# Kernel optimization log

Measured on AMD Instinct MI355X. Metric: run time of the kernel, lower is better.

The kernel has to match this reference:

```python
import jax, jax.numpy as jnp
import numpy as np

N = 170000      # nodes
E = 2400000     # edges
F_IN = 128      # dataset.num_features
H = 64          # hidden_channels
C = 40          # dataset.num_classes
L = 8           # num_layers
ENTROPY = 1.0   # args.entropy
EPS = 1e-20


def setup_inputs() -> dict:
    key = jax.random.key(0)
    ks = jax.random.split(key, 10)
    x = jax.random.normal(ks[0], (N, F_IN), jnp.float32)
    edge_src = jax.random.randint(ks[1], (E,), 0, N)
    edge_dst = jax.random.randint(ks[2], (E,), 0, N)
    edge_weight = jax.random.uniform(ks[3], (E,), jnp.float32) / 14.0  # ~1/deg scale
    u = jax.random.uniform(ks[4], (N, L + 1), jnp.float32, 1e-6, 1.0 - 1e-6)
    gumbel = -jnp.log(-jnp.log(u))  # standard Gumbel noise for gumbel_softmax
    lin0_w = jax.random.normal(ks[5], (F_IN, H), jnp.float32) / np.float32(np.sqrt(F_IN))
    lin0_b = jnp.zeros((H,), jnp.float32)
    meta_w = jax.random.normal(ks[6], (H, 1), jnp.float32) / np.float32(np.sqrt(H))
    meta_b = jnp.zeros((1,), jnp.float32)
    lin1_w = jax.random.normal(ks[7], (H, C), jnp.float32) / np.float32(np.sqrt(H))
    lin1_b = jnp.zeros((C,), jnp.float32)
    return dict(x=x, edge_weight=edge_weight, gumbel=gumbel,
                lin0_w=lin0_w, lin0_b=lin0_b, meta_w=meta_w, meta_b=meta_b,
                lin1_w=lin1_w, lin1_b=lin1_b,
                edge_src=edge_src, edge_dst=edge_dst)


def reference(x, edge_weight, gumbel, lin0_w, lin0_b, meta_w, meta_b,
              lin1_w, lin1_b, edge_src, edge_dst):
    # input projection + relu (dropout=0 -> no-op)
    x = jnp.maximum(x @ lin0_w + lin0_b, 0.0)  # [N,H]
    xs = [x]
    # GCNII layers with conv.alpha = conv.beta = 0 -> pure edge-weighted
    # scatter-add propagation followed by relu.
    for _ in range(L):
        msg = edge_weight[:, None] * x[edge_src]              # [E,H] gather
        x = jax.ops.segment_sum(msg, edge_dst, num_segments=N)  # [N,H] scatter-add
        x = jnp.maximum(x, 0.0)
        xs.append(x)
    xMat = jnp.stack(xs, axis=1)  # [N, L+1, H] (preds == xMatrix since concat='none')
    # MetaNet: [N, L+1]
    r = jnp.squeeze(xMat @ meta_w, -1) + meta_b[0]
    # get_t: stick-breaking with sigmoid; last column uses t=1 times cumprod
    s = jax.nn.sigmoid(r)                                    # [N, L+1]
    cp_excl = jnp.concatenate(
        [jnp.ones((N, 1), s.dtype), jnp.cumprod(1.0 - s, axis=1)[:, :-1]], axis=1)
    t = s * cp_excl
    t = t.at[:, -1].set(cp_excl[:, -1])
    ent_loss = ENTROPY * (-(jnp.log(t + EPS) * t).sum(1).mean())
    # gumbel_softmax(log(t+eps), tau=1, hard=False)
    tM = jax.nn.softmax(jnp.log(t + EPS) + gumbel, axis=1)   # [N, L+1]
    # layer mixing: [N,1,L+1] @ [N,L+1,H] -> [N,H]
    out = jnp.einsum('nl,nlh->nh', tM, xMat)
    out = out @ lin1_w + lin1_b
    return jax.nn.log_softmax(out, axis=-1), ent_loss
```

## Files before the change

### kernel.cpp

```cpp
#include <hip/hip_runtime.h>
#include <hip/hip_bf16.h>

#define N_NODES 170000
#define N_EDGES 2400000
#define F_IN_   128
#define H_      64
#define C_OUT   40
#define L_LAYERS 8
#define LP1     9
#define EPS_T   1e-20f
#define ROW_ELEMS (LP1 * H_)

typedef unsigned short u16;

__device__ __forceinline__ float bf2f(u16 u) {
    union { unsigned int i; float f; } c; c.i = ((unsigned int)u) << 16; return c.f;
}
__device__ __forceinline__ u16 f2bf(float f) {
    __hip_bfloat16 h = __float2bfloat16(f);
    return *reinterpret_cast<u16*>(&h);
}

__device__ __forceinline__ float waveReduceSum(float v) {
    for (int m = 32; m; m >>= 1) v += __shfl_xor(v, m, 64);
    return v;
}
__device__ __forceinline__ float waveReduceMax(float v) {
    for (int m = 32; m; m >>= 1) v = fmaxf(v, __shfl_xor(v, m, 64));
    return v;
}

__global__ __launch_bounds__(256) void k_zero4(float4* __restrict__ p) {
    p[blockIdx.x * 256 + threadIdx.x] = make_float4(0.f, 0.f, 0.f, 0.f);
}

__global__ __launch_bounds__(256) void k_hist(
    const int* __restrict__ edst, int* __restrict__ deg)
{
    int e = blockIdx.x * 256 + threadIdx.x;
    if (e < N_EDGES) atomicAdd(&deg[edst[e]], 1);
}

#define SCAN_TPB 256
#define SCAN_VPT 8
#define SCAN_EPB (SCAN_TPB * SCAN_VPT)
#define SCAN_BLOCKS ((N_NODES + SCAN_EPB - 1) / SCAN_EPB)

__global__ __launch_bounds__(SCAN_TPB) void k_scan1(
    const int* __restrict__ deg, int* __restrict__ rowstart,
    int* __restrict__ blockSums)
{
    __shared__ int tsum[SCAN_TPB];
    int tid = threadIdx.x;
    int base = blockIdx.x * SCAN_EPB + tid * SCAN_VPT;
    int vals[SCAN_VPT];
    int local = 0;
    #pragma unroll
    for (int i = 0; i < SCAN_VPT; ++i) {
        int idx = base + i;
        int v = (idx < N_NODES) ? deg[idx] : 0;
        vals[i] = local;
        local += v;
    }
    tsum[tid] = local;
    __syncthreads();
    for (int off = 1; off < SCAN_TPB; off <<= 1) {
        int v = (tid >= off) ? tsum[tid - off] : 0;
        __syncthreads();
        tsum[tid] += v;
        __syncthreads();
    }
    int texcl = tsum[tid] - local;
    #pragma unroll
    for (int i = 0; i < SCAN_VPT; ++i) {
        int idx = base + i;
        if (idx < N_NODES) rowstart[idx] = texcl + vals[i];
    }
    if (tid == SCAN_TPB - 1) blockSums[blockIdx.x] = tsum[tid];
}

__global__ __launch_bounds__(64) void k_scan2(int* __restrict__ blockSums) {
    if (threadIdx.x == 0) {
        int acc = 0;
        for (int i = 0; i < SCAN_BLOCKS; ++i) {
            int v = blockSums[i];
            blockSums[i] = acc;
            acc += v;
        }
    }
}

__global__ __launch_bounds__(SCAN_TPB) void k_scan3(
    int* __restrict__ rowstart, const int* __restrict__ blockSums)
{
    int off = blockSums[blockIdx.x];
    int base = blockIdx.x * SCAN_EPB + threadIdx.x * SCAN_VPT;
    #pragma unroll
    for (int i = 0; i < SCAN_VPT; ++i) {
        int idx = base + i;
        if (idx < N_NODES) rowstart[idx] += off;
    }
}

__global__ __launch_bounds__(256) void k_bucket(
    const int* __restrict__ esrc, const int* __restrict__ edst,
    const float* __restrict__ ew, const int* __restrict__ rowstart,
    int* __restrict__ cursor, int2* __restrict__ csr, int lo, int hi)
{
    int e = blockIdx.x * 256 + threadIdx.x;
    if (e >= N_EDGES) return;
    int d = edst[e];
    if (d < lo || d >= hi) return;
    int p = rowstart[d] + atomicAdd(&cursor[d], 1);
    csr[p] = make_int2(esrc[e], __float_as_int(ew[e]));
}

#define L0_NPB 64
__global__ __launch_bounds__(256) void k_lin0(
    const float* __restrict__ x, const float* __restrict__ W0,
    const float* __restrict__ b0, const float* __restrict__ mw,
    const float* __restrict__ mb, u16* __restrict__ xMatB,
    float* __restrict__ r)
{
    __shared__ float Wt[H_ * F_IN_];
    __shared__ float xr[L0_NPB * F_IN_];
    int tid = threadIdx.x;
    for (int i = tid; i < F_IN_ * H_; i += 256) {
        int k = i >> 6, c = i & 63;
        Wt[c * F_IN_ + (k ^ ((c & 7) << 2))] = W0[i];
    }
    int nb = blockIdx.x * L0_NPB;
    const float4* x4 = (const float4*)(x + (size_t)nb * F_IN_);
    float4* xr4 = (float4*)xr;
    int nvalid = N_NODES - nb; if (nvalid > L0_NPB) nvalid = L0_NPB;
    int limit4 = nvalid * (F_IN_ / 4);
    for (int i = tid; i < L0_NPB * (F_IN_ / 4); i += 256)
        xr4[i] = (i < limit4) ? x4[i] : make_float4(0.f, 0.f, 0.f, 0.f);
    __syncthreads();

    int wave = tid >> 6, lane = tid & 63;
    const int mbase = wave * 16;
    float bias = b0[lane];
    float acc[16];
    #pragma unroll
    for (int j = 0; j < 16; ++j) acc[j] = bias;
    const int wrow = lane * F_IN_;
    const int wsw = (lane & 7) << 2;
    for (int k0 = 0; k0 < F_IN_; k0 += 4) {
        float4 wv = *(const float4*)&Wt[wrow + (k0 ^ wsw)];
        #pragma unroll
        for (int j = 0; j < 16; ++j) {
            float4 xv = *(const float4*)&xr[(mbase + j) * F_IN_ + k0];
            acc[j] = fmaf(xv.w, wv.w,
                     fmaf(xv.z, wv.z, fmaf(xv.y, wv.y, fmaf(xv.x, wv.x, acc[j]))));
        }
    }
    float mwv = mw[lane];
    for (int j = 0; j < 16; ++j) {
        int n = nb + mbase + j;
        if (n >= N_NODES) break;
        float v = fmaxf(acc[j], 0.f);
        xMatB[(size_t)n * ROW_ELEMS + lane] = f2bf(v);
        float pr = waveReduceSum(v * mwv);
        if (lane == 0) r[n * LP1] = pr + mb[0];
    }
}

__global__ __launch_bounds__(256) void k_prop(
    const u16* __restrict__ xMatB, int l,
    const int* __restrict__ rowstart, const int* __restrict__ deg,
    const int2* __restrict__ csr,
    const float* __restrict__ mw, const float* __restrict__ mb,
    u16* __restrict__ xMatOut, float* __restrict__ r)
{
    int tid = threadIdx.x, wave = tid >> 6, lane = tid & 63;
    int n = blockIdx.x * 4 + wave;
    int sl = lane & 15, q = lane >> 4;
    int start = rowstart[n];
    int d = deg[n];
    int dm1 = (d > 0) ? (d - 1) : 0;

    int myS = 0; float myW = 0.f;
    if (lane < d) {
        int2 e = csr[start + lane];
        myS = e.x; myW = __int_as_float(e.y);
    }
    const unsigned loff = (unsigned)l * H_ + sl * 4;

    float a0x = 0.f, a0y = 0.f, a0z = 0.f, a0w = 0.f;
    float a1x = 0.f, a1y = 0.f, a1z = 0.f, a1w = 0.f;
    float a2x = 0.f, a2y = 0.f, a2z = 0.f, a2w = 0.f;
    float a3x = 0.f, a3y = 0.f, a3z = 0.f, a3w = 0.f;

    int dmax = (d < 64) ? d : 64;
    int kb = 0;
    do {
        int idx0 = kb + q;
        int idx1 = kb + q + 4;
        int idx2 = kb + q + 8;
        int idx3 = kb + q + 12;
        int ic0 = (idx0 < dm1) ? idx0 : dm1;
        int ic1 = (idx1 < dm1) ? idx1 : dm1;
        int ic2 = (idx2 < dm1) ? idx2 : dm1;
        int ic3 = (idx3 < dm1) ? idx3 : dm1;
        int   s0 = __shfl(myS, ic0, 64); float w0 = __shfl(myW, ic0, 64);
        int   s1 = __shfl(myS, ic1, 64); float w1 = __shfl(myW, ic1, 64);
        int   s2 = __shfl(myS, ic2, 64); float w2 = __shfl(myW, ic2, 64);
        int   s3 = __shfl(myS, ic3, 64); float w3 = __shfl(myW, ic3, 64);
        if (idx0 >= d) w0 = 0.f;
        if (idx1 >= d) w1 = 0.f;
        if (idx2 >= d) w2 = 0.f;
        if (idx3 >= d) w3 = 0.f;
        ushort4 v0 = *reinterpret_cast<const ushort4*>(
            &xMatB[(size_t)(unsigned)s0 * ROW_ELEMS + loff]);
        ushort4 v1 = *reinterpret_cast<const ushort4*>(
            &xMatB[(size_t)(unsigned)s1 * ROW_ELEMS + loff]);
        ushort4 v2 = *reinterpret_cast<const ushort4*>(
            &xMatB[(size_t)(unsigned)s2 * ROW_ELEMS + loff]);
        ushort4 v3 = *reinterpret_cast<const ushort4*>(
            &xMatB[(size_t)(unsigned)s3 * ROW_ELEMS + loff]);
        a0x = fmaf(bf2f(v0.x), w0, a0x); a0y = fmaf(bf2f(v0.y), w0, a0y);
        a0z = fmaf(bf2f(v0.z), w0, a0z); a0w = fmaf(bf2f(v0.w), w0, a0w);
        a1x = fmaf(bf2f(v1.x), w1, a1x); a1y = fmaf(bf2f(v1.y), w1, a1y);
        a1z = fmaf(bf2f(v1.z), w1, a1z); a1w = fmaf(bf2f(v1.w), w1, a1w);
        a2x = fmaf(bf2f(v2.x), w2, a2x); a2y = fmaf(bf2f(v2.y), w2, a2y);
        a2z = fmaf(bf2f(v2.z), w2, a2z); a2w = fmaf(bf2f(v2.w), w2, a2w);
        a3x = fmaf(bf2f(v3.x), w3, a3x); a3y = fmaf(bf2f(v3.y), w3, a3y);
        a3z = fmaf(bf2f(v3.z), w3, a3z); a3w = fmaf(bf2f(v3.w), w3, a3w);
        kb += 16;
    } while (kb < dmax);

    for (int kb2 = 64; kb2 < d; kb2 += 16) {
        #pragma unroll
        for (int j = 0; j < 4; ++j) {
            int idx = kb2 + j * 4 + q;
            if (idx < d) {
                int2 e = csr[start + idx];
                float w = __int_as_float(e.y);
                ushort4 v = *reinterpret_cast<const ushort4*>(
                    &xMatB[(size_t)(unsigned)e.x * ROW_ELEMS + loff]);
                a0x = fmaf(bf2f(v.x), w, a0x);
                a0y = fmaf(bf2f(v.y), w, a0y);
                a0z = fmaf(bf2f(v.z), w, a0z);
                a0w = fmaf(bf2f(v.w), w, a0w);
            }
        }
    }

    float r0 = a0x + a1x + a2x + a3x;
    float r1 = a0y + a1y + a2y + a3y;
    float r2 = a0z + a1z + a2z + a3z;
    float r3 = a0w + a1w + a2w + a3w;
    r0 += __shfl_xor(r0, 16, 64); r0 += __shfl_xor(r0, 32, 64);
    r1 += __shfl_xor(r1, 16, 64); r1 += __shfl_xor(r1, 32, 64);
    r2 += __shfl_xor(r2, 16, 64); r2 += __shfl_xor(r2, 32, 64);
    r3 += __shfl_xor(r3, 16, 64); r3 += __shfl_xor(r3, 32, 64);
    r0 = fmaxf(r0, 0.f); r1 = fmaxf(r1, 0.f);
    r2 = fmaxf(r2, 0.f); r3 = fmaxf(r3, 0.f);
    if (q == 0) {
        ushort4 o; o.x = f2bf(r0); o.y = f2bf(r1); o.z = f2bf(r2); o.w = f2bf(r3);
        *reinterpret_cast<ushort4*>(
            &xMatOut[(size_t)n * ROW_ELEMS + (l + 1) * H_ + sl * 4]) = o;
    }
    float dot = r0 * mw[4 * sl] + r1 * mw[4 * sl + 1] +
                r2 * mw[4 * sl + 2] + r3 * mw[4 * sl + 3];
    dot += __shfl_xor(dot, 1, 64);
    dot += __shfl_xor(dot, 2, 64);
    dot += __shfl_xor(dot, 4, 64);
    dot += __shfl_xor(dot, 8, 64);
    if (lane == 0) r[n * LP1 + (l + 1)] = dot + mb[0];
}

__global__ __launch_bounds__(256) void k_gate(
    const float* __restrict__ r, const float* __restrict__ gum,
    float* __restrict__ tM, float* __restrict__ entPart)
{
    __shared__ float lds[4];
    int tid = threadIdx.x;
    int n = blockIdx.x * 256 + tid;
    float ent = 0.f;
    if (n < N_NODES) {
        float t[LP1], lg[LP1];
        float cp = 1.f;
        #pragma unroll
        for (int j = 0; j < LP1; ++j) {
            float rv = r[n * LP1 + j];
            float s = 1.f / (1.f + expf(-rv));
            t[j] = (j == L_LAYERS) ? cp : s * cp;
            cp *= (1.f - s);
        }
        float mx = -INFINITY;
        #pragma unroll
        for (int j = 0; j < LP1; ++j) {
            float lt = logf(t[j] + EPS_T);
            ent -= t[j] * lt;
            lg[j] = lt + gum[n * LP1 + j];
            mx = fmaxf(mx, lg[j]);
        }
        float se = 0.f;
        #pragma unroll
        for (int j = 0; j < LP1; ++j) { lg[j] = expf(lg[j] - mx); se += lg[j]; }
        float inv = 1.f / se;
        #pragma unroll
        for (int j = 0; j < LP1; ++j) tM[n * LP1 + j] = lg[j] * inv;
    }
    float s = waveReduceSum(ent);
    int wave = tid >> 6, lane = tid & 63;
    if (lane == 0) lds[wave] = s;
    __syncthreads();
    if (tid == 0) entPart[blockIdx.x] = lds[0] + lds[1] + lds[2] + lds[3];
}

__global__ __launch_bounds__(256) void k_final(
    const u16* __restrict__ xMatB, const float* __restrict__ tM,
    const float* __restrict__ W1, const float* __restrict__ b1,
    float* __restrict__ out)
{
    __shared__ float mixLds[4][H_];
    int tid = threadIdx.x, wave = tid >> 6, lane = tid & 63;
    int n = blockIdx.x * 4 + wave;
    float tm = (lane < LP1) ? tM[n * LP1 + lane] : 0.f;
    float m = 0.f;
    #pragma unroll
    for (int j = 0; j < LP1; ++j) {
        float w = __shfl(tm, j, 64);
        m = fmaf(w, bf2f(xMatB[(size_t)n * ROW_ELEMS + j * H_ + lane]), m);
    }
    mixLds[wave][lane] = m;
    __syncthreads();
    float o = -INFINITY;
    if (lane < C_OUT) {
        float a = b1[lane];
        #pragma unroll 8
        for (int h = 0; h < H_; ++h)
            a = fmaf(mixLds[wave][h], W1[h * C_OUT + lane], a);
        o = a;
    }
    float omx = waveReduceMax(o);
    float ex = (lane < C_OUT) ? expf(o - omx) : 0.f;
    float es = waveReduceSum(ex);
    if (lane < C_OUT)
        out[(size_t)n * C_OUT + lane] = o - omx - logf(es);
}

__global__ __launch_bounds__(256) void k_entreduce(
    const float* __restrict__ part, int n, float scale, float* __restrict__ out)
{
    __shared__ float lds[4];
    int tid = threadIdx.x;
    float s = 0.f;
    for (int i = tid; i < n; i += 256) s += part[i];
    s = waveReduceSum(s);
    int wave = tid >> 6, lane = tid & 63;
    if (lane == 0) lds[wave] = s;
    __syncthreads();
    if (tid == 0) out[0] = (lds[0] + lds[1] + lds[2] + lds[3]) * scale;
}

extern "C" void kernel_launch(void* const* d_in, const int* in_sizes, int n_in,
                              void* d_out, int out_size, void* d_ws, size_t ws_size,
                              hipStream_t stream)
{
    const float* x   = (const float*)d_in[0];
    const float* ew  = (const float*)d_in[1];
    const float* gum = (const float*)d_in[2];
    const float* W0  = (const float*)d_in[3];
    const float* b0  = (const float*)d_in[4];
    const float* mw  = (const float*)d_in[5];
    const float* mb  = (const float*)d_in[6];
    const float* W1  = (const float*)d_in[7];
    const float* b1  = (const float*)d_in[8];
    const int* esrc  = (const int*)d_in[9];
    const int* edst  = (const int*)d_in[10];
    float* out = (float*)d_out;

    const size_t xMatBytes = (size_t)N_NODES * ROW_ELEMS * sizeof(u16);
    const size_t rBytes    = (size_t)N_NODES * LP1 * sizeof(float);
    const size_t tMBytes   = (size_t)N_NODES * LP1 * sizeof(float);
    const size_t entBytes  = (size_t)((N_NODES + 255) / 256) * sizeof(float);
    const size_t degBytes  = (size_t)N_NODES * sizeof(int);
    const size_t curBytes  = (size_t)N_NODES * sizeof(int);
    const size_t rowBytes  = (size_t)N_NODES * sizeof(int);
    const size_t bsBytes   = 512;
    const size_t csrBytes  = (size_t)N_EDGES * sizeof(int2);
    const size_t need = xMatBytes + rBytes + tMBytes + entBytes + degBytes +
                        curBytes + rowBytes + bsBytes + csrBytes;
    if (ws_size < need) return;

    char* p = (char*)d_ws;
    u16*  xMatB    = (u16*)p;           p += xMatBytes;
    float* rbuf    = (float*)p;         p += rBytes;
    float* tMbuf   = (float*)p;         p += tMBytes;
    float* entP    = (float*)p;         p += entBytes;
    int*  deg      = (int*)p;           p += degBytes;
    int*  cursor   = (int*)p;           p += curBytes;
    int*  rowstart = (int*)p;           p += rowBytes;
    int*  blockSums= (int*)p;           p += bsBytes;
    int2* csr      = (int2*)p;

    const int nodeBlocks = N_NODES / 4;
    const int edgeBlocks = (N_EDGES + 255) / 256;
    const int gateBlocks = (N_NODES + 255) / 256;
    const int lin0Blocks = (N_NODES + L0_NPB - 1) / L0_NPB;

    k_zero4<<<333, 256, 0, stream>>>((float4*)deg);
    k_hist<<<edgeBlocks, 256, 0, stream>>>(edst, deg);
    k_scan1<<<SCAN_BLOCKS, SCAN_TPB, 0, stream>>>(deg, rowstart, blockSums);
    k_scan2<<<1, 64, 0, stream>>>(blockSums);
    k_scan3<<<SCAN_BLOCKS, SCAN_TPB, 0, stream>>>(rowstart, blockSums);
    const int STEP = N_NODES / 8;
    for (int i = 0; i < 8; ++i)
        k_bucket<<<edgeBlocks, 256, 0, stream>>>(esrc, edst, ew, rowstart,
                                                 cursor, csr, i * STEP,
                                                 (i + 1) * STEP);

    k_lin0<<<lin0Blocks, 256, 0, stream>>>(x, W0, b0, mw, mb, xMatB, rbuf);
    for (int l = 0; l < L_LAYERS; ++l)
        k_prop<<<nodeBlocks, 256, 0, stream>>>(xMatB, l, rowstart, deg, csr,
                                               mw, mb, xMatB, rbuf);
    k_gate<<<gateBlocks, 256, 0, stream>>>(rbuf, gum, tMbuf, entP);
    k_final<<<nodeBlocks, 256, 0, stream>>>(xMatB, tMbuf, W1, b1, out);
    k_entreduce<<<1, 256, 0, stream>>>(entP, gateBlocks, 1.0f / N_NODES,
                                       out + (size_t)N_NODES * C_OUT);
}
```

Before: 958.3 us.

## Compute input projection with bf16 MFMA instead of fp32 FMA

Rewrites the lin0 projection kernel to use 16x16x32 bf16 MFMA instructions. The weights are converted to bf16 in shared memory and held as register fragments, while x rows are read directly from global memory and converted to bf16 per lane. The relu, the store into the bf16 layer matrix and the meta-net dot product are fused into the MFMA epilogue. This removes the fp32 FMA inner loop and the shared-memory staging of x, at the cost of bf16 rounding of the inputs and weights and less coalesced global reads of x.

New measurement: 872.9 us. -8.9%, faster.

```diff
diff --git a/kernel.cpp b/kernel.cpp
--- a/kernel.cpp
+++ b/kernel.cpp
@@ -12,6 +12,8 @@
 #define ROW_ELEMS (LP1 * H_)
 
 typedef unsigned short u16;
+typedef short bf16x8 __attribute__((ext_vector_type(8)));
+typedef float f32x4 __attribute__((ext_vector_type(4)));
 
 __device__ __forceinline__ float bf2f(u16 u) {
     union { unsigned int i; float f; } c; c.i = ((unsigned int)u) << 16; return c.f;
@@ -115,54 +117,91 @@
     csr[p] = make_int2(esrc[e], __float_as_int(ew[e]));
 }
 
-#define L0_NPB 64
 __global__ __launch_bounds__(256) void k_lin0(
     const float* __restrict__ x, const float* __restrict__ W0,
     const float* __restrict__ b0, const float* __restrict__ mw,
     const float* __restrict__ mb, u16* __restrict__ xMatB,
     float* __restrict__ r)
 {
-    __shared__ float Wt[H_ * F_IN_];
-    __shared__ float xr[L0_NPB * F_IN_];
+    __shared__ u16 Wt[H_ * F_IN_];
     int tid = threadIdx.x;
     for (int i = tid; i < F_IN_ * H_; i += 256) {
         int k = i >> 6, c = i & 63;
-        Wt[c * F_IN_ + (k ^ ((c & 7) << 2))] = W0[i];
-    }
-    int nb = blockIdx.x * L0_NPB;
-    const float4* x4 = (const float4*)(x + (size_t)nb * F_IN_);
-    float4* xr4 = (float4*)xr;
-    int nvalid = N_NODES - nb; if (nvalid > L0_NPB) nvalid = L0_NPB;
-    int limit4 = nvalid * (F_IN_ / 4);
-    for (int i = tid; i < L0_NPB * (F_IN_ / 4); i += 256)
-        xr4[i] = (i < limit4) ? x4[i] : make_float4(0.f, 0.f, 0.f, 0.f);
+        Wt[c * F_IN_ + (k ^ ((c & 7) << 3))] = f2bf(W0[i]);
+    }
     __syncthreads();
 
     int wave = tid >> 6, lane = tid & 63;
-    const int mbase = wave * 16;
-    float bias = b0[lane];
-    float acc[16];
-    #pragma unroll
-    for (int j = 0; j < 16; ++j) acc[j] = bias;
-    const int wrow = lane * F_IN_;
-    const int wsw = (lane & 7) << 2;
-    for (int k0 = 0; k0 < F_IN_; k0 += 4) {
-        float4 wv = *(const float4*)&Wt[wrow + (k0 ^ wsw)];
-        #pragma unroll
-        for (int j = 0; j < 16; ++j) {
-            float4 xv = *(const float4*)&xr[(mbase + j) * F_IN_ + k0];
-            acc[j] = fmaf(xv.w, wv.w,
-                     fmaf(xv.z, wv.z, fmaf(xv.y, wv.y, fmaf(xv.x, wv.x, acc[j]))));
-        }
-    }
-    float mwv = mw[lane];
-    for (int j = 0; j < 16; ++j) {
-        int n = nb + mbase + j;
-        if (n >= N_NODES) break;
-        float v = fmaxf(acc[j], 0.f);
-        xMatB[(size_t)n * ROW_ELEMS + lane] = f2bf(v);
-        float pr = waveReduceSum(v * mwv);
-        if (lane == 0) r[n * LP1] = pr + mb[0];
+    int lg = lane >> 4;
+    int lr = lane & 15;
+
+    bf16x8 bfrag[4][4];
+    float b0v[4], mwv[4];
+    #pragma unroll
+    for (int ct = 0; ct < 4; ++ct) {
+        int c = ct * 16 + lr;
+        #pragma unroll
+        for (int kt = 0; kt < 4; ++kt) {
+            int kidx = (kt * 32 + lg * 8) ^ ((c & 7) << 3);
+            bfrag[ct][kt] = *reinterpret_cast<bf16x8*>(&Wt[c * F_IN_ + kidx]);
+        }
+        b0v[ct] = b0[c];
+        mwv[ct] = mw[c];
+    }
+    float mb0 = mb[0];
+
+    int nbase = blockIdx.x * 256 + wave * 64;
+    #pragma unroll
+    for (int m = 0; m < 4; ++m) {
+        int arow = nbase + m * 16 + lr;
+        int arowc = (arow < N_NODES) ? arow : (N_NODES - 1);
+        const float4* xrow = (const float4*)(x + (size_t)arowc * F_IN_);
+        f32x4 acc[4];
+        #pragma unroll
+        for (int ct = 0; ct < 4; ++ct) {
+            acc[ct][0] = b0v[ct]; acc[ct][1] = b0v[ct];
+            acc[ct][2] = b0v[ct]; acc[ct][3] = b0v[ct];
+        }
+        #pragma unroll
+        for (int kt = 0; kt < 4; ++kt) {
+            int k8 = kt * 8 + lg * 2;
+            float4 xa = xrow[k8];
+            float4 xb = xrow[k8 + 1];
+            bf16x8 a;
+            a[0] = (short)f2bf(xa.x); a[1] = (short)f2bf(xa.y);
+            a[2] = (short)f2bf(xa.z); a[3] = (short)f2bf(xa.w);
+            a[4] = (short)f2bf(xb.x); a[5] = (short)f2bf(xb.y);
+            a[6] = (short)f2bf(xb.z); a[7] = (short)f2bf(xb.w);
+            #pragma unroll
+            for (int ct = 0; ct < 4; ++ct)
+                acc[ct] = __builtin_amdgcn_mfma_f32_16x16x32_bf16(
+                    a, bfrag[ct][kt], acc[ct], 0, 0, 0);
+        }
+        float p[4];
+        #pragma unroll
+        for (int reg = 0; reg < 4; ++reg) {
+            int n = nbase + m * 16 + lg * 4 + reg;
+            float pr = 0.f;
+            #pragma unroll
+            for (int ct = 0; ct < 4; ++ct) {
+                float v = fmaxf(acc[ct][reg], 0.f);
+                if (n < N_NODES)
+                    xMatB[(size_t)n * ROW_ELEMS + ct * 16 + lr] = f2bf(v);
+                pr = fmaf(v, mwv[ct], pr);
+            }
+            p[reg] = pr;
+        }
+        #pragma unroll
+        for (int reg = 0; reg < 4; ++reg) {
+            p[reg] += __shfl_xor(p[reg], 1, 64);
+            p[reg] += __shfl_xor(p[reg], 2, 64);
+            p[reg] += __shfl_xor(p[reg], 4, 64);
+            p[reg] += __shfl_xor(p[reg], 8, 64);
+        }
+        if (lr < 4) {
+            int n = nbase + m * 16 + lg * 4 + lr;
+            if (n < N_NODES) r[n * LP1] = p[lr] + mb0;
+        }
     }
 }
 
@@ -401,7 +440,7 @@
     const int nodeBlocks = N_NODES / 4;
     const int edgeBlocks = (N_EDGES + 255) / 256;
     const int gateBlocks = (N_NODES + 255) / 256;
-    const int lin0Blocks = (N_NODES + L0_NPB - 1) / L0_NPB;
+    const int lin0Blocks = (N_NODES + 255) / 256;
 
     k_zero4<<<333, 256, 0, stream>>>((float4*)deg);
     k_hist<<<edgeBlocks, 256, 0, stream>>>(edst, deg);
```
